# Optimization experiments

Measured on AMD Instinct MI355X. Metric: run time of the kernel, lower is better.

Reference implementation:

```python
import jax, jax.numpy as jnp
import numpy as np

U, B, I, D = 50000, 20000, 40000, 64
E_UI, E_UB, E_UBX, E_AGG = 1000000, 600000, 800000, 300000
EPS = 1e-8


def _bip_graph(rng, nA, nB, nE):
    """Symmetric Laplacian-normalized bipartite graph as directed COO edge list."""
    r = rng.integers(0, nA, nE)
    c = rng.integers(0, nB, nE)
    deg_r = np.bincount(r, minlength=nA).astype(np.float32)
    deg_c = np.bincount(c, minlength=nB).astype(np.float32)
    v = (1.0 / (np.sqrt(deg_r[r]) + EPS)) * (1.0 / (np.sqrt(deg_c[c]) + EPS))
    rows = np.concatenate([r, c + nA])
    cols = np.concatenate([c + nA, r])
    vals = np.concatenate([v, v]).astype(np.float32)
    return np.stack([rows, cols]).astype(np.int32), vals


def setup_inputs() -> dict:
    rng = np.random.default_rng(0)
    ui_idx, ui_val = _bip_graph(rng, U, I, E_UI)
    ub_idx, ub_val = _bip_graph(rng, U, B, E_UB)
    ubx_idx, ubx_val = _bip_graph(rng, U, B, E_UBX)  # ingredient-augmented u-b graph
    # bundle aggregation graph: row-normalized B x I (bi graph)
    br = rng.integers(0, B, E_AGG)
    bc = rng.integers(0, I, E_AGG)
    bdeg = np.bincount(br, minlength=B).astype(np.float32)
    agg_val = (1.0 / np.maximum(bdeg[br], 1.0)).astype(np.float32)
    agg_idx = np.stack([br, bc]).astype(np.int32)
    key = jax.random.key(0)
    ku, kb, ki = jax.random.split(key, 3)
    s = np.sqrt(2.0 / (U + D)).astype(np.float32)  # xavier-normal-ish scale
    return {
        "users_feature": jax.random.normal(ku, (U, D), jnp.float32) * 0.02,
        "bundles_feature": jax.random.normal(kb, (B, D), jnp.float32) * 0.02,
        "items_feature": jax.random.normal(ki, (I, D), jnp.float32) * 0.02,
        "ui_idx": jnp.asarray(ui_idx), "ui_val": jnp.asarray(ui_val),
        "ub_idx": jnp.asarray(ub_idx), "ub_val": jnp.asarray(ub_val),
        "ubx_idx": jnp.asarray(ubx_idx), "ubx_val": jnp.asarray(ubx_val),
        "agg_idx": jnp.asarray(agg_idx), "agg_val": jnp.asarray(agg_val),
        "num_layers": 2,
    }


def _spmm(idx, val, x, n_out):
    # y[r] += val[e] * x[c] for each edge e=(r,c)
    return jax.ops.segment_sum(val[:, None] * x[idx[1]], idx[0], num_segments=n_out)


def _l2norm(x):
    n = jnp.sqrt(jnp.sum(x * x, axis=1, keepdims=True))
    return x / jnp.maximum(n, 1e-12)


def _one_propagate(idx, val, A_feat, B_feat, num_layers):
    feats = jnp.concatenate([A_feat, B_feat], axis=0)
    n = feats.shape[0]
    acc = feats  # layer 0 raw
    f = feats
    for i in range(num_layers):
        f = _spmm(idx, val, f, n) / (i + 2)
        acc = acc + _l2norm(f)
    return acc[: A_feat.shape[0]], acc[A_feat.shape[0]:]


def reference(users_feature, bundles_feature, items_feature, ui_idx, ui_val,
              ub_idx, ub_val, ubx_idx, ubx_val, agg_idx, agg_val, num_layers):
    # item-level propagation over user-item graph
    IL_u, IL_i = _one_propagate(ui_idx, ui_val, users_feature, items_feature, num_layers)
    IL_b = _spmm(agg_idx, agg_val, IL_i, bundles_feature.shape[0])  # bundle agg from items
    # bundle-level propagation over user-bundle graph
    BL_u, BL_b = _one_propagate(ub_idx, ub_val, users_feature, bundles_feature, num_layers)
    # ingredient-augmented user-bundle propagation
    XL_u, XL_b = _one_propagate(ubx_idx, ubx_val, users_feature, bundles_feature, num_layers)
    # pack all representations: [3*U + 3*B, D]
    return jnp.concatenate([IL_u, BL_u, XL_u, IL_b, BL_b, XL_b], axis=0)
```

## Files before the change

### kernel.cpp

```cpp
#include <hip/hip_runtime.h>

#define D 64
constexpr int U_ = 50000, B_ = 20000, I_ = 40000;
constexpr int RPB  = 128;
constexpr int MAXB = 708;
constexpr int PTILE = 8192;

constexpr int NBU = 390;
constexpr int CAPU_UI = 3584, CAPB_UI = 4352;
constexpr int CAPA    = 2560;
constexpr int CAPU_UB = 2432, CAPB_UB = 4864;
constexpr int CAPU_UX = 2944, CAPB_UX = 6272;

__device__ __forceinline__ int g_nbU(int seg) { return seg == 1 ? 0 : NBU; }
__device__ __forceinline__ int g_capU(int seg) {
    switch (seg) { case 0: return CAPU_UI; case 1: return CAPA;
                   case 2: return CAPU_UB; default: return CAPU_UX; }
}
__device__ __forceinline__ int g_capB(int seg) {
    switch (seg) { case 0: return CAPB_UI; case 1: return CAPA;
                   case 2: return CAPB_UB; default: return CAPB_UX; }
}
__device__ __forceinline__ int bbase(int seg, int b) {
    int nbU = g_nbU(seg);
    return (b <= nbU) ? b * g_capU(seg)
                      : nbU * g_capU(seg) + (b - nbU) * g_capB(seg);
}

__device__ __forceinline__ unsigned short f2bf(float f) {
    unsigned int u = __float_as_uint(f);
    return (unsigned short)((u + 0x7FFFu + ((u >> 16) & 1u)) >> 16);
}

struct BuildP {
    const int *r0, *r1, *r2, *r3;
    int nnz0, nnz1, nnz2, nnz3;
    int G0, G1, G2, G3;
    int nb0, nb1, nb2, nb3;
    int co0, co1, co2, co3;
};

__global__ void __launch_bounds__(256)
k_cnt4(BuildP p, int* __restrict__ cnt) {
    __shared__ int lcnt[MAXB];
    int blk = blockIdx.x, t = threadIdx.x;
    int seg, rel, nnz, G, nbuck, co; const int* rows;
    if (blk < p.G0)                   { seg=0; rel=blk;              rows=p.r0; nnz=p.nnz0; G=p.G0; nbuck=p.nb0; co=p.co0; }
    else if (blk < p.G0+p.G1)         { seg=1; rel=blk-p.G0;         rows=p.r1; nnz=p.nnz1; G=p.G1; nbuck=p.nb1; co=p.co1; }
    else if (blk < p.G0+p.G1+p.G2)    { seg=2; rel=blk-p.G0-p.G1;    rows=p.r2; nnz=p.nnz2; G=p.G2; nbuck=p.nb2; co=p.co2; }
    else                              { seg=3; rel=blk-p.G0-p.G1-p.G2; rows=p.r3; nnz=p.nnz3; G=p.G3; nbuck=p.nb3; co=p.co3; }
    (void)seg;
    for (int i = t; i < nbuck; i += 256) lcnt[i] = 0;
    __syncthreads();
    int e0 = rel * PTILE, e1 = min(e0 + PTILE, nnz);
    int e = e0 + t;
    for (; e + 1792 < e1; e += 2048) {
        int r[8];
        #pragma unroll
        for (int k = 0; k < 8; k++) r[k] = rows[e + k * 256];
        #pragma unroll
        for (int k = 0; k < 8; k++) atomicAdd(&lcnt[r[k] >> 7], 1);
    }
    for (; e < e1; e += 256) atomicAdd(&lcnt[rows[e] >> 7], 1);
    __syncthreads();
    for (int b = t; b < nbuck; b += 256) cnt[co + (size_t)b * G + rel] = lcnt[b];
}

__global__ void __launch_bounds__(256)
k_scan4(BuildP p, int* __restrict__ cnt, int* __restrict__ bktcur) {
    __shared__ int sv[256];
    int bk = blockIdx.x, t = threadIdx.x;
    int seg, rel, G, co;
    if (bk < p.nb0)                    { seg=0; rel=bk;                 G=p.G0; co=p.co0; }
    else if (bk < p.nb0+p.nb1)         { seg=1; rel=bk-p.nb0;           G=p.G1; co=p.co1; }
    else if (bk < p.nb0+p.nb1+p.nb2)   { seg=2; rel=bk-p.nb0-p.nb1;     G=p.G2; co=p.co2; }
    else                               { seg=3; rel=bk-p.nb0-p.nb1-p.nb2; G=p.G3; co=p.co3; }
    int x = (t < G) ? cnt[co + (size_t)rel * G + t] : 0;
    sv[t] = x;
    __syncthreads();
    for (int off = 1; off < 256; off <<= 1) {
        int y = (t >= off) ? sv[t - off] : 0;
        __syncthreads();
        sv[t] += y;
        __syncthreads();
    }
    int bb = bbase(seg, rel);
    if (t < G) cnt[co + (size_t)rel * G + t] = bb + sv[t] - x;
    if (t == 255) bktcur[seg * MAXB + rel] = bb + sv[255];
}

__global__ void __launch_bounds__(256)
k_scat(const int* __restrict__ rows, const int* __restrict__ cols,
       int nnz, int G, int nbuck, int seg,
       const int* __restrict__ cnt, int* __restrict__ ep) {
    __shared__ int lbase[MAXB], lcnt[MAXB], llim[MAXB];
    int t = threadIdx.x, blk = blockIdx.x;
    for (int b = t; b < nbuck; b += 256) {
        lbase[b] = cnt[(size_t)b * G + blk];
        llim[b]  = bbase(seg, b + 1);
        lcnt[b]  = 0;
    }
    __syncthreads();
    int e0 = blk * PTILE, e1 = min(e0 + PTILE, nnz);
    int e = e0 + t;
    for (; e + 1792 < e1; e += 2048) {
        int r[8], c[8];
        #pragma unroll
        for (int k = 0; k < 8; k++) { r[k] = rows[e + k * 256]; c[k] = cols[e + k * 256]; }
        #pragma unroll
        for (int k = 0; k < 8; k++) {
            int b = r[k] >> 7;
            int pos = lbase[b] + atomicAdd(&lcnt[b], 1);
            if (pos < llim[b])
                ep[pos] = ((r[k] & (RPB - 1)) << 17) | c[k];
        }
    }
    for (; e < e1; e += 256) {
        int r = rows[e], c = cols[e];
        int b = r >> 7;
        int pos = lbase[b] + atomicAdd(&lcnt[b], 1);
        if (pos < llim[b])
            ep[pos] = ((r & (RPB - 1)) << 17) | c;
    }
}

__global__ void __launch_bounds__(256)
k_sort(const int* __restrict__ ep, const int* __restrict__ bktcur, int seg,
       int n, int mode, int do_pad, int* __restrict__ ecolS,
       int* __restrict__ rowstart, int* __restrict__ rowend,
       float* __restrict__ scale, int do_stage,
       const float* __restrict__ rawA, const float* __restrict__ rawB_adj,
       ushort* __restrict__ fb) {
    __shared__ int lc[4 * 129];
    __shared__ float sscale[RPB];
    __shared__ int wtot;
    int t = threadIdx.x;
    int b = blockIdx.x;
    int s = bbase(seg, b);
    int e = min(bktcur[b], bbase(seg, b + 1));
    int ne = e - s;
    for (int i = t; i < 4 * 129; i += 256) lc[i] = 0;
    __syncthreads();
    int rep = (t & 3) * 129;
    int i = t;
    for (; i + 768 < ne; i += 1024) {
        int p0 = ep[s + i], p1 = ep[s + i + 256], p2 = ep[s + i + 512], p3 = ep[s + i + 768];
        atomicAdd(&lc[rep + (p0 >> 17)], 1); atomicAdd(&lc[rep + (p1 >> 17)], 1);
        atomicAdd(&lc[rep + (p2 >> 17)], 1); atomicAdd(&lc[rep + (p3 >> 17)], 1);
    }
    for (; i < ne; i += 256) { int p = ep[s + i]; atomicAdd(&lc[rep + (p >> 17)], 1); }
    __syncthreads();
    int c_t = 0, pc_t = 0, v = 0;
    if (t < RPB) {
        c_t = lc[t] + lc[129 + t] + lc[258 + t] + lc[387 + t];
        pc_t = do_pad ? ((c_t + 7) & ~7) : c_t;
        v = pc_t;
        for (int off = 1; off < 64; off <<= 1) {
            int y = __shfl_up(v, off, 64);
            if ((t & 63) >= off) v += y;
        }
    }
    if (t == 63) wtot = v;
    __syncthreads();
    if (t >= 64 && t < RPB) v += wtot;
    if (t < RPB) {
        int row = b * RPB + t;
        if (row < n) {
            int st = s + (v - pc_t);
            rowstart[row] = st;
            rowend[row]   = st + pc_t;
            float sc = (mode == 0) ? 1.0f / (sqrtf((float)c_t) + 1e-8f)
                                   : 1.0f / (float)max(c_t, 1);
            scale[row] = sc;
            sscale[t] = sc;
            for (int k = c_t; k < pc_t; k++) ecolS[st + k] = n;
            lc[t] = st;
        } else lc[t] = 0;
    }
    __syncthreads();
    i = t;
    for (; i + 768 < ne; i += 1024) {
        int p0 = ep[s + i], p1 = ep[s + i + 256], p2 = ep[s + i + 512], p3 = ep[s + i + 768];
        int q0 = atomicAdd(&lc[p0 >> 17], 1); ecolS[q0] = p0 & 0x1FFFF;
        int q1 = atomicAdd(&lc[p1 >> 17], 1); ecolS[q1] = p1 & 0x1FFFF;
        int q2 = atomicAdd(&lc[p2 >> 17], 1); ecolS[q2] = p2 & 0x1FFFF;
        int q3 = atomicAdd(&lc[p3 >> 17], 1); ecolS[q3] = p3 & 0x1FFFF;
    }
    for (; i < ne; i += 256) {
        int p = ep[s + i];
        int q = atomicAdd(&lc[p >> 17], 1);
        ecolS[q] = p & 0x1FFFF;
    }
    if (do_stage) {
        int r0 = b * RPB;
        for (int idx = t; idx < RPB * 16; idx += 256) {
            int rl = idx >> 4, q = idx & 15;
            int row = r0 + rl;
            if (row > n) continue;
            ushort4 o;
            if (row == n) {
                o = make_ushort4(0, 0, 0, 0);
            } else {
                float sc = sscale[rl];
                float4 vv = (row < U_) ? ((const float4*)rawA)[(size_t)row * 16 + q]
                                       : ((const float4*)rawB_adj)[(size_t)row * 16 + q];
                o.x = f2bf(vv.x * sc); o.y = f2bf(vv.y * sc);
                o.z = f2bf(vv.z * sc); o.w = f2bf(vv.w * sc);
            }
            ((ushort4*)fb)[(size_t)row * 16 + q] = o;
        }
    }
}

__global__ void __launch_bounds__(256)
k_layer(const int* __restrict__ rowstart, const int* __restrict__ rowend,
        const int* __restrict__ ecol,
        const float* __restrict__ scale, int n, int zrow,
        const ushort* __restrict__ x, float inv,
        const float* __restrict__ rawA, const float* __restrict__ rawB_adj,
        ushort* __restrict__ fout, int write_f, int init,
        float* __restrict__ accA, float* __restrict__ accB) {
    if (write_f && blockIdx.x == 0 && threadIdx.x < 16)
        ((ushort4*)(fout + ((size_t)zrow << 6)))[threadIdx.x] = make_ushort4(0, 0, 0, 0);
    const int lane = threadIdx.x & 63;
    const int qtr  = lane >> 4;
    const int ql   = lane & 15;
    const int g = ql >> 3, q = ql & 7;
    int rowA = (blockIdx.x << 4) + ((threadIdx.x >> 6) << 2);
    if (rowA >= n) return;
    int row = rowA + qtr;
    int s = 0, e = 0;
    if (row < n) { s = rowstart[row]; e = rowend[row]; }
    float a0=0.f,a1=0.f,a2=0.f,a3=0.f,a4=0.f,a5=0.f,a6=0.f,a7=0.f;
    const uint4* __restrict__ xb = (const uint4*)x;

#define LDQ(m, vv) { int c_ = __shfl(cj, (qtr << 4) + ((m) << 1) + g, 64); \
                     vv = xb[((size_t)(unsigned)c_ << 3) + (unsigned)q]; }
#define ACCQ(vv) { \
    a0 += __uint_as_float(vv.x << 16); a1 += __uint_as_float(vv.x & 0xFFFF0000u); \
    a2 += __uint_as_float(vv.y << 16); a3 += __uint_as_float(vv.y & 0xFFFF0000u); \
    a4 += __uint_as_float(vv.z << 16); a5 += __uint_as_float(vv.z & 0xFFFF0000u); \
    a6 += __uint_as_float(vv.w << 16); a7 += __uint_as_float(vv.w & 0xFFFF0000u); }

    for (int base = s; base < e; base += 16) {
        int jn = e - base;
        int cj = ecol[base + ql];
        uint4 v0, v1, v2, v3, v4, v5, v6, v7;
        if (jn >= 16) {
            LDQ(0, v0); LDQ(1, v1); LDQ(2, v2); LDQ(3, v3);
            LDQ(4, v4); ACCQ(v0);
            LDQ(5, v5); ACCQ(v1);
            LDQ(6, v6); ACCQ(v2);
            LDQ(7, v7); ACCQ(v3);
            ACCQ(v4); ACCQ(v5); ACCQ(v6); ACCQ(v7);
        } else {
            LDQ(0, v0); LDQ(1, v1); LDQ(2, v2); LDQ(3, v3);
            ACCQ(v0); ACCQ(v1); ACCQ(v2); ACCQ(v3);
        }
    }
#undef LDQ
#undef ACCQ
#define RED(aa) { aa += __shfl_xor(aa, 8, 64); }
    RED(a0) RED(a1) RED(a2) RED(a3) RED(a4) RED(a5) RED(a6) RED(a7)
#undef RED
    float srow = (row < n) ? scale[row] : 0.f;
    float mlt = srow * inv;
    float w0=a0*mlt, w1=a1*mlt, w2=a2*mlt, w3=a3*mlt;
    float w4=a4*mlt, w5=a5*mlt, w6=a6*mlt, w7=a7*mlt;
    float sq = w0*w0 + w1*w1 + w2*w2 + w3*w3 + w4*w4 + w5*w5 + w6*w6 + w7*w7;
    sq += __shfl_xor(sq, 1, 64); sq += __shfl_xor(sq, 2, 64); sq += __shfl_xor(sq, 4, 64);
    float rn = 1.0f / fmaxf(sqrtf(sq), 1e-12f);
    if (row < n && g == 0) {
        size_t o = ((size_t)row << 6) + ((unsigned)q << 3);
        if (write_f) {
            unsigned p0 = (unsigned)f2bf(w0*srow) | ((unsigned)f2bf(w1*srow) << 16);
            unsigned p1 = (unsigned)f2bf(w2*srow) | ((unsigned)f2bf(w3*srow) << 16);
            unsigned p2 = (unsigned)f2bf(w4*srow) | ((unsigned)f2bf(w5*srow) << 16);
            unsigned p3 = (unsigned)f2bf(w6*srow) | ((unsigned)f2bf(w7*srow) << 16);
            *(uint4*)(fout + o) = make_uint4(p0, p1, p2, p3);
        }
        float r0=w0*rn, r1=w1*rn, r2=w2*rn, r3=w3*rn;
        float r4=w4*rn, r5=w5*rn, r6=w6*rn, r7=w7*rn;
        float* p = (row < U_) ? accA + o : accB + (o - ((size_t)U_ << 6));
        float4 c0, c1;
        if (init) {
            const float4* rp = (const float4*)((row < U_) ? rawA : rawB_adj)
                               + ((size_t)row << 4) + ((unsigned)q << 1);
            c0 = rp[0]; c1 = rp[1];
        } else {
            c0 = ((const float4*)p)[0]; c1 = ((const float4*)p)[1];
        }
        ((float4*)p)[0] = make_float4(c0.x + r0, c0.y + r1, c0.z + r2, c0.w + r3);
        ((float4*)p)[1] = make_float4(c1.x + r4, c1.y + r5, c1.z + r6, c1.w + r7);
    }
}

__global__ void k_spmm_csr(const int* __restrict__ rowstart, const int* __restrict__ rowend,
                           const int* __restrict__ ecol,
                           const float* __restrict__ rs, int n,
                           const float* __restrict__ x, float* __restrict__ y) {
    int row = (blockIdx.x << 2) + (threadIdx.x >> 6);
    if (row >= n) return;
    int lane = threadIdx.x & 63;
    int s = rowstart[row], e = rowend[row];
    float acc = 0.f;
    for (int base = s; base < e; base += 64) {
        int jn = e - base; if (jn > 64) jn = 64;
        int li = base + (lane < jn ? lane : jn - 1);
        int cj = ecol[li];
        int j = 0;
        for (; j + 8 <= jn; j += 8) {
            int c0 = __shfl(cj, j + 0, 64), c1 = __shfl(cj, j + 1, 64);
            int c2 = __shfl(cj, j + 2, 64), c3 = __shfl(cj, j + 3, 64);
            int c4 = __shfl(cj, j + 4, 64), c5 = __shfl(cj, j + 5, 64);
            int c6 = __shfl(cj, j + 6, 64), c7 = __shfl(cj, j + 7, 64);
            float v0 = x[(size_t)c0 * D + lane], v1 = x[(size_t)c1 * D + lane];
            float v2 = x[(size_t)c2 * D + lane], v3 = x[(size_t)c3 * D + lane];
            float v4 = x[(size_t)c4 * D + lane], v5 = x[(size_t)c5 * D + lane];
            float v6 = x[(size_t)c6 * D + lane], v7 = x[(size_t)c7 * D + lane];
            acc += ((v0 + v1) + (v2 + v3)) + ((v4 + v5) + (v6 + v7));
        }
        for (; j < jn; j++) {
            int c = __shfl(cj, j, 64);
            acc += x[(size_t)c * D + lane];
        }
    }
    y[(size_t)row * D + lane] = acc * rs[row];
}

extern "C" void kernel_launch(void* const* d_in, const int* in_sizes, int n_in,
                              void* d_out, int out_size, void* d_ws, size_t ws_size,
                              hipStream_t stream) {
    const float* users   = (const float*)d_in[0];
    const float* bundles = (const float*)d_in[1];
    const float* items   = (const float*)d_in[2];
    const int*   ui_idx  = (const int*)d_in[3];
    const int*   ub_idx  = (const int*)d_in[5];
    const int*   ubx_idx = (const int*)d_in[7];
    const int*   agg_idx = (const int*)d_in[9];
    const int ui_nnz  = in_sizes[4];
    const int ub_nnz  = in_sizes[6];
    const int ubx_nnz = in_sizes[8];
    const int agg_nnz = in_sizes[10];

    float* out = (float*)d_out;
    const size_t rowf = (size_t)D;

    const int NROWPAD = 90004;
    const int EPMAX   = 547 * 6144;
    ushort* fb16    = (ushort*)d_ws;
    float*  acc_itm = (float*)(fb16 + (size_t)(90001) * D + 32);
    float*  scale   = acc_itm + (size_t)I_ * D;
    int*    ep      = (int*)(scale + NROWPAD);
    ushort* gb16    = (ushort*)ep;
    int*    ecolS   = ep + EPMAX;
    int*    rowstart= ecolS + EPMAX;
    int*    rowend  = rowstart + NROWPAD;
    int*    bktcur  = rowend + NROWPAD;
    int*    cnt     = ep + 2950000;

    float* out_IL_u = out;
    float* out_BL_u = out + (size_t)U_ * rowf;
    float* out_XL_u = out + (size_t)2 * U_ * rowf;
    float* out_IL_b = out + (size_t)3 * U_ * rowf;
    float* out_BL_b = out + (size_t)3 * U_ * rowf + (size_t)B_ * rowf;
    float* out_XL_b = out + (size_t)3 * U_ * rowf + (size_t)2 * B_ * rowf;

    BuildP P;
    P.r0 = ui_idx;  P.nnz0 = ui_nnz;  P.G0 = (ui_nnz  + PTILE - 1) / PTILE;  P.nb0 = 704;
    P.r1 = agg_idx; P.nnz1 = agg_nnz; P.G1 = (agg_nnz + PTILE - 1) / PTILE;  P.nb1 = 157;
    P.r2 = ub_idx;  P.nnz2 = ub_nnz;  P.G2 = (ub_nnz  + PTILE - 1) / PTILE;  P.nb2 = 547;
    P.r3 = ubx_idx; P.nnz3 = ubx_nnz; P.G3 = (ubx_nnz + PTILE - 1) / PTILE;  P.nb3 = 547;
    P.co0 = 0;
    P.co1 = P.co0 + P.nb0 * P.G0;
    P.co2 = P.co1 + P.nb1 * P.G1;
    P.co3 = P.co2 + P.nb2 * P.G2;
    int Gsum  = P.G0 + P.G1 + P.G2 + P.G3;
    int nbsum = P.nb0 + P.nb1 + P.nb2 + P.nb3;
    hipLaunchKernelGGL(k_cnt4,  dim3(Gsum),  dim3(256), 0, stream, P, cnt);
    hipLaunchKernelGGL(k_scan4, dim3(nbsum), dim3(256), 0, stream, P, cnt, bktcur);

    auto build = [&](const int* idxp, int nnz, int n, int mode, int do_pad,
                     int do_stage, const float* A, const float* Badj,
                     int seg, int G, int co) {
        int nbuck = (n + RPB - 1) / RPB;
        hipLaunchKernelGGL(k_scat, dim3(G), dim3(256), 0, stream,
                           idxp, idxp + nnz, nnz, G, nbuck, seg, cnt + co, ep);
        hipLaunchKernelGGL(k_sort, dim3(nbuck), dim3(256), 0, stream,
                           ep, bktcur + seg * MAXB, seg, n, mode, do_pad, ecolS,
                           rowstart, rowend, scale, do_stage, A, Badj, fb16);
    };

    auto propagate = [&](const int* idxp, int nnz, int seg, int G, int co,
                         const float* Bfeat, int nB, float* accA, float* accB) {
        const int n = U_ + nB;
        const float* Badj = Bfeat - (size_t)U_ * rowf;
        build(idxp, nnz, n, 0, 1, 1, users, Badj, seg, G, co);
        hipLaunchKernelGGL(k_layer, dim3((n + 15) / 16), dim3(256), 0, stream,
                           rowstart, rowend, ecolS, scale, n, n, fb16, 0.5f,
                           users, Badj, gb16, 1, 1, accA, accB);
        hipLaunchKernelGGL(k_layer, dim3((n + 15) / 16), dim3(256), 0, stream,
                           rowstart, rowend, ecolS, scale, n, n, gb16, 1.0f / 3.0f,
                           users, Badj, (ushort*)nullptr, 0, 0, accA, accB);
    };

    propagate(ui_idx, ui_nnz, 0, P.G0, P.co0, items, I_, out_IL_u, acc_itm);

    build(agg_idx, agg_nnz, B_, 1, 0, 0, users, users, 1, P.G1, P.co1);
    hipLaunchKernelGGL(k_spmm_csr, dim3((B_ + 3) / 4), dim3(256), 0, stream,
                       rowstart, rowend, ecolS, scale, B_, acc_itm, out_IL_b);

    propagate(ub_idx, ub_nnz, 2, P.G2, P.co2, bundles, B_, out_BL_u, out_BL_b);

    propagate(ubx_idx, ubx_nnz, 3, P.G3, P.co3, bundles, B_, out_XL_u, out_XL_b);
}
```

Baseline: 463.3 us.

## Batch all four graph builds and propagations into combined multi-graph launches

Gives each graph its own workspace regions, so that the scatter, sort and layer kernels for all graphs can run as single grouped launches instead of a serialized per-graph sequence. The kernel count drops from about 17 to 8, which removes launch gaps and lets small grids fill the GPU. The cost is a larger workspace, plus a per-block search to find which graph the block belongs to. When the workspace is too small, the code falls back to the old per-graph sequence.

```diff
diff --git a/kernel.cpp b/kernel.cpp
--- a/kernel.cpp
+++ b/kernel.cpp
@@ -11,6 +11,11 @@
 constexpr int CAPA    = 2560;
 constexpr int CAPU_UB = 2432, CAPB_UB = 4864;
 constexpr int CAPU_UX = 2944, CAPB_UX = 6272;
+constexpr int EXT_UI = NBU * CAPU_UI + 314 * CAPB_UI;
+constexpr int EXT_AG = 157 * CAPA;
+constexpr int EXT_UB = NBU * CAPU_UB + 157 * CAPB_UB;
+constexpr int EXT_UX = NBU * CAPU_UX + 157 * CAPB_UX;
+constexpr long long EXT_SUM = (long long)EXT_UI + EXT_AG + EXT_UB + EXT_UX;
 
 __device__ __forceinline__ int g_nbU(int seg) { return seg == 1 ? 0 : NBU; }
 __device__ __forceinline__ int g_capU(int seg) {
@@ -32,27 +37,27 @@
     return (unsigned short)((u + 0x7FFFu + ((u >> 16) & 1u)) >> 16);
 }
 
-struct BuildP {
-    const int *r0, *r1, *r2, *r3;
-    int nnz0, nnz1, nnz2, nnz3;
-    int G0, G1, G2, G3;
-    int nb0, nb1, nb2, nb3;
-    int co0, co1, co2, co3;
+struct GD {
+    const int* rows; const int* cols;
+    int* ep; int* cnt; int* bktcur;
+    int* ecol; int* rowstart; int* rowend; float* scale;
+    const float* rawA; const float* rawB_adj;
+    ushort* fb;
+    int nnz, G, nbuck, seg, n, mode, do_pad, do_stage;
 };
-
-__global__ void __launch_bounds__(256)
-k_cnt4(BuildP p, int* __restrict__ cnt) {
+struct GB4 { GD g[4]; int ng; int Gpre[5]; int nbpre[5]; };
+
+__global__ void __launch_bounds__(256) k_cntB(GB4 P) {
     __shared__ int lcnt[MAXB];
     int blk = blockIdx.x, t = threadIdx.x;
-    int seg, rel, nnz, G, nbuck, co; const int* rows;
-    if (blk < p.G0)                   { seg=0; rel=blk;              rows=p.r0; nnz=p.nnz0; G=p.G0; nbuck=p.nb0; co=p.co0; }
-    else if (blk < p.G0+p.G1)         { seg=1; rel=blk-p.G0;         rows=p.r1; nnz=p.nnz1; G=p.G1; nbuck=p.nb1; co=p.co1; }
-    else if (blk < p.G0+p.G1+p.G2)    { seg=2; rel=blk-p.G0-p.G1;    rows=p.r2; nnz=p.nnz2; G=p.G2; nbuck=p.nb2; co=p.co2; }
-    else                              { seg=3; rel=blk-p.G0-p.G1-p.G2; rows=p.r3; nnz=p.nnz3; G=p.G3; nbuck=p.nb3; co=p.co3; }
-    (void)seg;
-    for (int i = t; i < nbuck; i += 256) lcnt[i] = 0;
-    __syncthreads();
-    int e0 = rel * PTILE, e1 = min(e0 + PTILE, nnz);
+    int gi = 0;
+    while (gi + 1 < P.ng && blk >= P.Gpre[gi + 1]) gi++;
+    const GD& d = P.g[gi];
+    int rel = blk - P.Gpre[gi];
+    const int* __restrict__ rows = d.rows;
+    for (int i = t; i < d.nbuck; i += 256) lcnt[i] = 0;
+    __syncthreads();
+    int e0 = rel * PTILE, e1 = min(e0 + PTILE, d.nnz);
     int e = e0 + t;
     for (; e + 1792 < e1; e += 2048) {
         int r[8];
@@ -63,19 +68,17 @@
     }
     for (; e < e1; e += 256) atomicAdd(&lcnt[rows[e] >> 7], 1);
     __syncthreads();
-    for (int b = t; b < nbuck; b += 256) cnt[co + (size_t)b * G + rel] = lcnt[b];
-}
-
-__global__ void __launch_bounds__(256)
-k_scan4(BuildP p, int* __restrict__ cnt, int* __restrict__ bktcur) {
+    for (int b = t; b < d.nbuck; b += 256) d.cnt[(size_t)b * d.G + rel] = lcnt[b];
+}
+
+__global__ void __launch_bounds__(256) k_scanB(GB4 P) {
     __shared__ int sv[256];
     int bk = blockIdx.x, t = threadIdx.x;
-    int seg, rel, G, co;
-    if (bk < p.nb0)                    { seg=0; rel=bk;                 G=p.G0; co=p.co0; }
-    else if (bk < p.nb0+p.nb1)         { seg=1; rel=bk-p.nb0;           G=p.G1; co=p.co1; }
-    else if (bk < p.nb0+p.nb1+p.nb2)   { seg=2; rel=bk-p.nb0-p.nb1;     G=p.G2; co=p.co2; }
-    else                               { seg=3; rel=bk-p.nb0-p.nb1-p.nb2; G=p.G3; co=p.co3; }
-    int x = (t < G) ? cnt[co + (size_t)rel * G + t] : 0;
+    int gi = 0;
+    while (gi + 1 < P.ng && bk >= P.nbpre[gi + 1]) gi++;
+    const GD& d = P.g[gi];
+    int rel = bk - P.nbpre[gi];
+    int x = (t < d.G) ? d.cnt[(size_t)rel * d.G + t] : 0;
     sv[t] = x;
     __syncthreads();
     for (int off = 1; off < 256; off <<= 1) {
@@ -84,24 +87,28 @@
         sv[t] += y;
         __syncthreads();
     }
-    int bb = bbase(seg, rel);
-    if (t < G) cnt[co + (size_t)rel * G + t] = bb + sv[t] - x;
-    if (t == 255) bktcur[seg * MAXB + rel] = bb + sv[255];
-}
-
-__global__ void __launch_bounds__(256)
-k_scat(const int* __restrict__ rows, const int* __restrict__ cols,
-       int nnz, int G, int nbuck, int seg,
-       const int* __restrict__ cnt, int* __restrict__ ep) {
+    int bb = bbase(d.seg, rel);
+    if (t < d.G) d.cnt[(size_t)rel * d.G + t] = bb + sv[t] - x;
+    if (t == 255) d.bktcur[rel] = bb + sv[255];
+}
+
+__global__ void __launch_bounds__(256) k_scatB(GB4 P) {
     __shared__ int lbase[MAXB], lcnt[MAXB], llim[MAXB];
-    int t = threadIdx.x, blk = blockIdx.x;
-    for (int b = t; b < nbuck; b += 256) {
-        lbase[b] = cnt[(size_t)b * G + blk];
-        llim[b]  = bbase(seg, b + 1);
+    int blk = blockIdx.x, t = threadIdx.x;
+    int gi = 0;
+    while (gi + 1 < P.ng && blk >= P.Gpre[gi + 1]) gi++;
+    const GD& d = P.g[gi];
+    int rel = blk - P.Gpre[gi];
+    const int* __restrict__ rows = d.rows;
+    const int* __restrict__ cols = d.cols;
+    int* __restrict__ ep = d.ep;
+    for (int b = t; b < d.nbuck; b += 256) {
+        lbase[b] = d.cnt[(size_t)b * d.G + rel];
+        llim[b]  = bbase(d.seg, b + 1);
         lcnt[b]  = 0;
     }
     __syncthreads();
-    int e0 = blk * PTILE, e1 = min(e0 + PTILE, nnz);
+    int e0 = rel * PTILE, e1 = min(e0 + PTILE, d.nnz);
     int e = e0 + t;
     for (; e + 1792 < e1; e += 2048) {
         int r[8], c[8];
@@ -124,27 +131,26 @@
     }
 }
 
-__global__ void __launch_bounds__(256)
-k_sort(const int* __restrict__ ep, const int* __restrict__ bktcur, int seg,
-       int n, int mode, int do_pad, int* __restrict__ ecolS,
-       int* __restrict__ rowstart, int* __restrict__ rowend,
-       float* __restrict__ scale, int do_stage,
-       const float* __restrict__ rawA, const float* __restrict__ rawB_adj,
-       ushort* __restrict__ fb) {
+__global__ void __launch_bounds__(256) k_sortB(GB4 P) {
     __shared__ int lc[4 * 129];
     __shared__ float sscale[RPB];
     __shared__ int wtot;
-    int t = threadIdx.x;
-    int b = blockIdx.x;
-    int s = bbase(seg, b);
-    int e = min(bktcur[b], bbase(seg, b + 1));
+    int bk = blockIdx.x, t = threadIdx.x;
+    int gi = 0;
+    while (gi + 1 < P.ng && bk >= P.nbpre[gi + 1]) gi++;
+    const GD& d = P.g[gi];
+    int b = bk - P.nbpre[gi];
+    const int* __restrict__ ep = d.ep;
+    int* __restrict__ ecol = d.ecol;
+    int s = bbase(d.seg, b);
+    int e = min(d.bktcur[b], bbase(d.seg, b + 1));
     int ne = e - s;
     for (int i = t; i < 4 * 129; i += 256) lc[i] = 0;
     __syncthreads();
     int rep = (t & 3) * 129;
     int i = t;
     for (; i + 768 < ne; i += 1024) {
-        int p0 = ep[s + i], p1 = ep[s + i + 256], p2 = ep[s + i + 512], p3 = ep[s + i + 768];
+        int p0 = ep[s+i], p1 = ep[s+i+256], p2 = ep[s+i+512], p3 = ep[s+i+768];
         atomicAdd(&lc[rep + (p0 >> 17)], 1); atomicAdd(&lc[rep + (p1 >> 17)], 1);
         atomicAdd(&lc[rep + (p2 >> 17)], 1); atomicAdd(&lc[rep + (p3 >> 17)], 1);
     }
@@ -153,7 +159,7 @@
     int c_t = 0, pc_t = 0, v = 0;
     if (t < RPB) {
         c_t = lc[t] + lc[129 + t] + lc[258 + t] + lc[387 + t];
-        pc_t = do_pad ? ((c_t + 7) & ~7) : c_t;
+        pc_t = d.do_pad ? ((c_t + 7) & ~7) : c_t;
         v = pc_t;
         for (int off = 1; off < 64; off <<= 1) {
             int y = __shfl_up(v, off, 64);
@@ -165,75 +171,85 @@
     if (t >= 64 && t < RPB) v += wtot;
     if (t < RPB) {
         int row = b * RPB + t;
-        if (row < n) {
+        if (row < d.n) {
             int st = s + (v - pc_t);
-            rowstart[row] = st;
-            rowend[row]   = st + pc_t;
-            float sc = (mode == 0) ? 1.0f / (sqrtf((float)c_t) + 1e-8f)
-                                   : 1.0f / (float)max(c_t, 1);
-            scale[row] = sc;
+            d.rowstart[row] = st;
+            d.rowend[row]   = st + pc_t;
+            float sc = (d.mode == 0) ? 1.0f / (sqrtf((float)c_t) + 1e-8f)
+                                     : 1.0f / (float)max(c_t, 1);
+            d.scale[row] = sc;
             sscale[t] = sc;
-            for (int k = c_t; k < pc_t; k++) ecolS[st + k] = n;
+            for (int k = c_t; k < pc_t; k++) ecol[st + k] = d.n;
             lc[t] = st;
         } else lc[t] = 0;
     }
     __syncthreads();
     i = t;
     for (; i + 768 < ne; i += 1024) {
-        int p0 = ep[s + i], p1 = ep[s + i + 256], p2 = ep[s + i + 512], p3 = ep[s + i + 768];
-        int q0 = atomicAdd(&lc[p0 >> 17], 1); ecolS[q0] = p0 & 0x1FFFF;
-        int q1 = atomicAdd(&lc[p1 >> 17], 1); ecolS[q1] = p1 & 0x1FFFF;
-        int q2 = atomicAdd(&lc[p2 >> 17], 1); ecolS[q2] = p2 & 0x1FFFF;
-        int q3 = atomicAdd(&lc[p3 >> 17], 1); ecolS[q3] = p3 & 0x1FFFF;
+        int p0 = ep[s+i], p1 = ep[s+i+256], p2 = ep[s+i+512], p3 = ep[s+i+768];
+        int q0 = atomicAdd(&lc[p0 >> 17], 1); ecol[q0] = p0 & 0x1FFFF;
+        int q1 = atomicAdd(&lc[p1 >> 17], 1); ecol[q1] = p1 & 0x1FFFF;
+        int q2 = atomicAdd(&lc[p2 >> 17], 1); ecol[q2] = p2 & 0x1FFFF;
+        int q3 = atomicAdd(&lc[p3 >> 17], 1); ecol[q3] = p3 & 0x1FFFF;
     }
     for (; i < ne; i += 256) {
         int p = ep[s + i];
         int q = atomicAdd(&lc[p >> 17], 1);
-        ecolS[q] = p & 0x1FFFF;
-    }
-    if (do_stage) {
+        ecol[q] = p & 0x1FFFF;
+    }
+    if (d.do_stage) {
         int r0 = b * RPB;
         for (int idx = t; idx < RPB * 16; idx += 256) {
             int rl = idx >> 4, q = idx & 15;
             int row = r0 + rl;
-            if (row > n) continue;
+            if (row > d.n) continue;
             ushort4 o;
-            if (row == n) {
+            if (row == d.n) {
                 o = make_ushort4(0, 0, 0, 0);
             } else {
                 float sc = sscale[rl];
-                float4 vv = (row < U_) ? ((const float4*)rawA)[(size_t)row * 16 + q]
-                                       : ((const float4*)rawB_adj)[(size_t)row * 16 + q];
+                float4 vv = (row < U_) ? ((const float4*)d.rawA)[(size_t)row * 16 + q]
+                                       : ((const float4*)d.rawB_adj)[(size_t)row * 16 + q];
                 o.x = f2bf(vv.x * sc); o.y = f2bf(vv.y * sc);
                 o.z = f2bf(vv.z * sc); o.w = f2bf(vv.w * sc);
             }
-            ((ushort4*)fb)[(size_t)row * 16 + q] = o;
-        }
-    }
-}
-
-__global__ void __launch_bounds__(256)
-k_layer(const int* __restrict__ rowstart, const int* __restrict__ rowend,
-        const int* __restrict__ ecol,
-        const float* __restrict__ scale, int n, int zrow,
-        const ushort* __restrict__ x, float inv,
-        const float* __restrict__ rawA, const float* __restrict__ rawB_adj,
-        ushort* __restrict__ fout, int write_f, int init,
-        float* __restrict__ accA, float* __restrict__ accB) {
-    if (write_f && blockIdx.x == 0 && threadIdx.x < 16)
-        ((ushort4*)(fout + ((size_t)zrow << 6)))[threadIdx.x] = make_ushort4(0, 0, 0, 0);
+            ((ushort4*)d.fb)[(size_t)row * 16 + q] = o;
+        }
+    }
+}
+
+struct LD {
+    const int* rowstart; const int* rowend; const float* scale;
+    const int* ecol; const ushort* x; ushort* fout;
+    const float* rawA; const float* rawB_adj;
+    float* accA; float* accB;
+    float inv; int n, write_f, init;
+};
+struct LB3 { LD l[3]; int nl; int qpre[4]; };
+
+__global__ void __launch_bounds__(256) k_layerB(LB3 P) {
+    int blk = blockIdx.x;
+    int gi = 0;
+    while (gi + 1 < P.nl && blk >= P.qpre[gi + 1]) gi++;
+    const LD& d = P.l[gi];
+    int rel = blk - P.qpre[gi];
+    if (d.write_f && rel == 0 && threadIdx.x < 16)
+        ((ushort4*)(d.fout + ((size_t)d.n << 6)))[threadIdx.x] = make_ushort4(0, 0, 0, 0);
+    const int* __restrict__ rowstart = d.rowstart;
+    const int* __restrict__ rowend   = d.rowend;
+    const int* __restrict__ ecol     = d.ecol;
+    const float* __restrict__ scale  = d.scale;
+    const uint4* __restrict__ xb = (const uint4*)d.x;
     const int lane = threadIdx.x & 63;
     const int qtr  = lane >> 4;
     const int ql   = lane & 15;
     const int g = ql >> 3, q = ql & 7;
-    int rowA = (blockIdx.x << 4) + ((threadIdx.x >> 6) << 2);
-    if (rowA >= n) return;
+    int rowA = (rel << 4) + ((threadIdx.x >> 6) << 2);
+    if (rowA >= d.n) return;
     int row = rowA + qtr;
     int s = 0, e = 0;
-    if (row < n) { s = rowstart[row]; e = rowend[row]; }
+    if (row < d.n) { s = rowstart[row]; e = rowend[row]; }
     float a0=0.f,a1=0.f,a2=0.f,a3=0.f,a4=0.f,a5=0.f,a6=0.f,a7=0.f;
-    const uint4* __restrict__ xb = (const uint4*)x;
-
 #define LDQ(m, vv) { int c_ = __shfl(cj, (qtr << 4) + ((m) << 1) + g, 64); \
                      vv = xb[((size_t)(unsigned)c_ << 3) + (unsigned)q]; }
 #define ACCQ(vv) { \
@@ -241,7 +257,6 @@
     a2 += __uint_as_float(vv.y << 16); a3 += __uint_as_float(vv.y & 0xFFFF0000u); \
     a4 += __uint_as_float(vv.z << 16); a5 += __uint_as_float(vv.z & 0xFFFF0000u); \
     a6 += __uint_as_float(vv.w << 16); a7 += __uint_as_float(vv.w & 0xFFFF0000u); }
-
     for (int base = s; base < e; base += 16) {
         int jn = e - base;
         int cj = ecol[base + ql];
@@ -263,28 +278,28 @@
 #define RED(aa) { aa += __shfl_xor(aa, 8, 64); }
     RED(a0) RED(a1) RED(a2) RED(a3) RED(a4) RED(a5) RED(a6) RED(a7)
 #undef RED
-    float srow = (row < n) ? scale[row] : 0.f;
-    float mlt = srow * inv;
+    float srow = (row < d.n) ? scale[row] : 0.f;
+    float mlt = srow * d.inv;
     float w0=a0*mlt, w1=a1*mlt, w2=a2*mlt, w3=a3*mlt;
     float w4=a4*mlt, w5=a5*mlt, w6=a6*mlt, w7=a7*mlt;
     float sq = w0*w0 + w1*w1 + w2*w2 + w3*w3 + w4*w4 + w5*w5 + w6*w6 + w7*w7;
     sq += __shfl_xor(sq, 1, 64); sq += __shfl_xor(sq, 2, 64); sq += __shfl_xor(sq, 4, 64);
     float rn = 1.0f / fmaxf(sqrtf(sq), 1e-12f);
-    if (row < n && g == 0) {
+    if (row < d.n && g == 0) {
         size_t o = ((size_t)row << 6) + ((unsigned)q << 3);
-        if (write_f) {
+        if (d.write_f) {
             unsigned p0 = (unsigned)f2bf(w0*srow) | ((unsigned)f2bf(w1*srow) << 16);
             unsigned p1 = (unsigned)f2bf(w2*srow) | ((unsigned)f2bf(w3*srow) << 16);
             unsigned p2 = (unsigned)f2bf(w4*srow) | ((unsigned)f2bf(w5*srow) << 16);
             unsigned p3 = (unsigned)f2bf(w6*srow) | ((unsigned)f2bf(w7*srow) << 16);
-            *(uint4*)(fout + o) = make_uint4(p0, p1, p2, p3);
+            *(uint4*)(d.fout + o) = make_uint4(p0, p1, p2, p3);
         }
         float r0=w0*rn, r1=w1*rn, r2=w2*rn, r3=w3*rn;
         float r4=w4*rn, r5=w5*rn, r6=w6*rn, r7=w7*rn;
-        float* p = (row < U_) ? accA + o : accB + (o - ((size_t)U_ << 6));
+        float* p = (row < U_) ? d.accA + o : d.accB + (o - ((size_t)U_ << 6));
         float4 c0, c1;
-        if (init) {
-            const float4* rp = (const float4*)((row < U_) ? rawA : rawB_adj)
+        if (d.init) {
+            const float4* rp = (const float4*)((row < U_) ? d.rawA : d.rawB_adj)
                                + ((size_t)row << 4) + ((unsigned)q << 1);
             c0 = rp[0]; c1 = rp[1];
         } else {
@@ -345,20 +360,6 @@
 
     float* out = (float*)d_out;
     const size_t rowf = (size_t)D;
-
-    const int NROWPAD = 90004;
-    const int EPMAX   = 547 * 6144;
-    ushort* fb16    = (ushort*)d_ws;
-    float*  acc_itm = (float*)(fb16 + (size_t)(90001) * D + 32);
-    float*  scale   = acc_itm + (size_t)I_ * D;
-    int*    ep      = (int*)(scale + NROWPAD);
-    ushort* gb16    = (ushort*)ep;
-    int*    ecolS   = ep + EPMAX;
-    int*    rowstart= ecolS + EPMAX;
-    int*    rowend  = rowstart + NROWPAD;
-    int*    bktcur  = rowend + NROWPAD;
-    int*    cnt     = ep + 2950000;
-
     float* out_IL_u = out;
     float* out_BL_u = out + (size_t)U_ * rowf;
     float* out_XL_u = out + (size_t)2 * U_ * rowf;
@@ -366,51 +367,158 @@
     float* out_BL_b = out + (size_t)3 * U_ * rowf + (size_t)B_ * rowf;
     float* out_XL_b = out + (size_t)3 * U_ * rowf + (size_t)2 * B_ * rowf;
 
-    BuildP P;
-    P.r0 = ui_idx;  P.nnz0 = ui_nnz;  P.G0 = (ui_nnz  + PTILE - 1) / PTILE;  P.nb0 = 704;
-    P.r1 = agg_idx; P.nnz1 = agg_nnz; P.G1 = (agg_nnz + PTILE - 1) / PTILE;  P.nb1 = 157;
-    P.r2 = ub_idx;  P.nnz2 = ub_nnz;  P.G2 = (ub_nnz  + PTILE - 1) / PTILE;  P.nb2 = 547;
-    P.r3 = ubx_idx; P.nnz3 = ubx_nnz; P.G3 = (ubx_nnz + PTILE - 1) / PTILE;  P.nb3 = 547;
-    P.co0 = 0;
-    P.co1 = P.co0 + P.nb0 * P.G0;
-    P.co2 = P.co1 + P.nb1 * P.G1;
-    P.co3 = P.co2 + P.nb2 * P.G2;
-    int Gsum  = P.G0 + P.G1 + P.G2 + P.G3;
-    int nbsum = P.nb0 + P.nb1 + P.nb2 + P.nb3;
-    hipLaunchKernelGGL(k_cnt4,  dim3(Gsum),  dim3(256), 0, stream, P, cnt);
-    hipLaunchKernelGGL(k_scan4, dim3(nbsum), dim3(256), 0, stream, P, cnt, bktcur);
-
-    auto build = [&](const int* idxp, int nnz, int n, int mode, int do_pad,
-                     int do_stage, const float* A, const float* Badj,
-                     int seg, int G, int co) {
-        int nbuck = (n + RPB - 1) / RPB;
-        hipLaunchKernelGGL(k_scat, dim3(G), dim3(256), 0, stream,
-                           idxp, idxp + nnz, nnz, G, nbuck, seg, cnt + co, ep);
-        hipLaunchKernelGGL(k_sort, dim3(nbuck), dim3(256), 0, stream,
-                           ep, bktcur + seg * MAXB, seg, n, mode, do_pad, ecolS,
-                           rowstart, rowend, scale, do_stage, A, Badj, fb16);
-    };
-
-    auto propagate = [&](const int* idxp, int nnz, int seg, int G, int co,
-                         const float* Bfeat, int nB, float* accA, float* accB) {
-        const int n = U_ + nB;
-        const float* Badj = Bfeat - (size_t)U_ * rowf;
-        build(idxp, nnz, n, 0, 1, 1, users, Badj, seg, G, co);
-        hipLaunchKernelGGL(k_layer, dim3((n + 15) / 16), dim3(256), 0, stream,
-                           rowstart, rowend, ecolS, scale, n, n, fb16, 0.5f,
-                           users, Badj, gb16, 1, 1, accA, accB);
-        hipLaunchKernelGGL(k_layer, dim3((n + 15) / 16), dim3(256), 0, stream,
-                           rowstart, rowend, ecolS, scale, n, n, gb16, 1.0f / 3.0f,
-                           users, Badj, (ushort*)nullptr, 0, 0, accA, accB);
-    };
-
-    propagate(ui_idx, ui_nnz, 0, P.G0, P.co0, items, I_, out_IL_u, acc_itm);
-
-    build(agg_idx, agg_nnz, B_, 1, 0, 0, users, users, 1, P.G1, P.co1);
-    hipLaunchKernelGGL(k_spmm_csr, dim3((B_ + 3) / 4), dim3(256), 0, stream,
-                       rowstart, rowend, ecolS, scale, B_, acc_itm, out_IL_b);
-
-    propagate(ub_idx, ub_nnz, 2, P.G2, P.co2, bundles, B_, out_BL_u, out_BL_b);
-
-    propagate(ubx_idx, ubx_nnz, 3, P.G3, P.co3, bundles, B_, out_XL_u, out_XL_b);
-}
+    const int G0 = (ui_nnz  + PTILE - 1) / PTILE;
+    const int G1 = (agg_nnz + PTILE - 1) / PTILE;
+    const int G2 = (ub_nnz  + PTILE - 1) / PTILE;
+    const int G3 = (ubx_nnz + PTILE - 1) / PTILE;
+    const int NB0 = 704, NB1 = 157, NB2 = 547, NB3 = 547;
+    const size_t co0 = 0, co1 = (size_t)NB0 * G0, co2 = co1 + (size_t)NB1 * G1,
+                 co3 = co2 + (size_t)NB2 * G2, cntInts = co3 + (size_t)NB3 * G3;
+    const int nU = U_ + I_, nB2g = U_ + B_;
+
+    const int* rowsArr[4] = { ui_idx, agg_idx, ub_idx, ubx_idx };
+    const int nnzArr[4]   = { ui_nnz, agg_nnz, ub_nnz, ubx_nnz };
+    const int GArr[4]     = { G0, G1, G2, G3 };
+    const int nbArr[4]    = { NB0, NB1, NB2, NB3 };
+    const int nArr[4]     = { nU, B_, nB2g, nB2g };
+    const int modeArr[4]  = { 0, 1, 0, 0 };
+    const int padArr[4]   = { 1, 0, 1, 1 };
+    const int stgArr[4]   = { 1, 0, 1, 1 };
+    const size_t coArr[4] = { co0, co1, co2, co3 };
+    const float* rawBArr[4] = { items - (size_t)U_ * rowf, users,
+                                bundles - (size_t)U_ * rowf, bundles - (size_t)U_ * rowf };
+
+    const size_t fbBytes  = 230003ull * 128;
+    const size_t accBytes = 40001ull * 256;
+    const size_t ecBytes  = (size_t)EXT_SUM * 4;
+    const size_t rsBytes  = 250016ull * 4;
+    const size_t bkBytes  = 4ull * MAXB * 4;
+    const size_t epcnt    = (size_t)EXT_SUM * 4 + cntInts * 4;
+    const size_t tailB    = epcnt > fbBytes ? epcnt : fbBytes;
+    const size_t reqA     = fbBytes + accBytes + ecBytes + 3 * rsBytes + bkBytes + tailB + 4096;
+
+    GB4 P{};
+    P.ng = 4;
+    P.Gpre[0] = 0; P.nbpre[0] = 0;
+    for (int i = 0; i < 4; i++) { P.Gpre[i+1] = P.Gpre[i] + GArr[i]; P.nbpre[i+1] = P.nbpre[i] + nbArr[i]; }
+
+    if (ws_size >= reqA) {
+        char* w = (char*)d_ws;
+        ushort* fbA   = (ushort*)w;                 w += fbBytes;
+        float* accI   = (float*)w;                  w += accBytes;
+        int*   ecolA  = (int*)w;                    w += ecBytes;
+        int*   rsA    = (int*)w;                    w += rsBytes;
+        int*   reA    = (int*)w;                    w += rsBytes;
+        float* scA    = (float*)w;                  w += rsBytes;
+        int*   bkA    = (int*)w;                    w += bkBytes;
+        int*   epA    = (int*)w;
+        int*   cntA   = epA + EXT_SUM;
+        ushort* gbA   = (ushort*)epA;
+
+        const size_t epoff[4] = { 0, (size_t)EXT_UI, (size_t)EXT_UI + EXT_AG,
+                                  (size_t)EXT_UI + EXT_AG + EXT_UB };
+        const size_t roff[4]  = { 0, 90004, 110008, 180012 };
+        const size_t fboff[4] = { 0, 0, 90001ull * 64, 160002ull * 64 };
+
+        for (int i = 0; i < 4; i++) {
+            GD& d = P.g[i];
+            d.rows = rowsArr[i]; d.cols = rowsArr[i] + nnzArr[i];
+            d.ep = epA + epoff[i]; d.cnt = cntA + coArr[i]; d.bktcur = bkA + i * MAXB;
+            d.ecol = ecolA + epoff[i];
+            d.rowstart = rsA + roff[i]; d.rowend = reA + roff[i]; d.scale = scA + roff[i];
+            d.rawA = users; d.rawB_adj = rawBArr[i];
+            d.fb = (i == 1) ? nullptr : fbA + fboff[i];
+            d.nnz = nnzArr[i]; d.G = GArr[i]; d.nbuck = nbArr[i]; d.seg = i;
+            d.n = nArr[i]; d.mode = modeArr[i]; d.do_pad = padArr[i]; d.do_stage = stgArr[i];
+        }
+        hipLaunchKernelGGL(k_cntB,  dim3(P.Gpre[4]),  dim3(256), 0, stream, P);
+        hipLaunchKernelGGL(k_scanB, dim3(P.nbpre[4]), dim3(256), 0, stream, P);
+        hipLaunchKernelGGL(k_scatB, dim3(P.Gpre[4]),  dim3(256), 0, stream, P);
+        hipLaunchKernelGGL(k_sortB, dim3(P.nbpre[4]), dim3(256), 0, stream, P);
+
+        float* accAArr[3] = { out_IL_u, out_BL_u, out_XL_u };
+        float* accBArr[3] = { accI, out_BL_b, out_XL_b };
+        int gsel[3] = { 0, 2, 3 };
+        LB3 L{};
+        L.nl = 3; L.qpre[0] = 0;
+        for (int j = 0; j < 3; j++) {
+            int i = gsel[j];
+            LD& l = L.l[j];
+            l.rowstart = P.g[i].rowstart; l.rowend = P.g[i].rowend; l.scale = P.g[i].scale;
+            l.ecol = P.g[i].ecol; l.rawA = users; l.rawB_adj = rawBArr[i];
+            l.accA = accAArr[j]; l.accB = accBArr[j];
+            l.n = nArr[i];
+            L.qpre[j + 1] = L.qpre[j] + ((nArr[i] + 15) >> 4);
+        }
+        for (int j = 0; j < 3; j++) {
+            int i = gsel[j];
+            L.l[j].x = fbA + fboff[i]; L.l[j].fout = gbA + fboff[i];
+            L.l[j].inv = 0.5f; L.l[j].write_f = 1; L.l[j].init = 1;
+        }
+        hipLaunchKernelGGL(k_layerB, dim3(L.qpre[3]), dim3(256), 0, stream, L);
+        for (int j = 0; j < 3; j++) {
+            int i = gsel[j];
+            L.l[j].x = gbA + fboff[i]; L.l[j].fout = (ushort*)nullptr;
+            L.l[j].inv = 1.0f / 3.0f; L.l[j].write_f = 0; L.l[j].init = 0;
+        }
+        hipLaunchKernelGGL(k_layerB, dim3(L.qpre[3]), dim3(256), 0, stream, L);
+        hipLaunchKernelGGL(k_spmm_csr, dim3((B_ + 3) / 4), dim3(256), 0, stream,
+                           P.g[1].rowstart, P.g[1].rowend, P.g[1].ecol,
+                           P.g[1].scale, B_, accI, out_IL_b);
+    } else {
+        const int NROWPAD = 90004;
+        const int EPMAX = 547 * 6144;
+        ushort* fb16 = (ushort*)d_ws;
+        float* accI  = (float*)(fb16 + (size_t)90001 * D + 32);
+        float* scB   = accI + (size_t)I_ * D;
+        int* epB     = (int*)(scB + NROWPAD);
+        ushort* gb16 = (ushort*)epB;
+        int* ecolB   = epB + EPMAX;
+        int* rsB     = ecolB + EPMAX;
+        int* reB     = rsB + NROWPAD;
+        int* bkB     = reB + NROWPAD;
+        int* cntB    = epB + 2950000;
+
+        for (int i = 0; i < 4; i++) {
+            GD& d = P.g[i];
+            d.rows = rowsArr[i]; d.cols = rowsArr[i] + nnzArr[i];
+            d.ep = epB; d.cnt = cntB + coArr[i]; d.bktcur = bkB + i * MAXB;
+            d.ecol = ecolB; d.rowstart = rsB; d.rowend = reB; d.scale = scB;
+            d.rawA = users; d.rawB_adj = rawBArr[i];
+            d.fb = fb16;
+            d.nnz = nnzArr[i]; d.G = GArr[i]; d.nbuck = nbArr[i]; d.seg = i;
+            d.n = nArr[i]; d.mode = modeArr[i]; d.do_pad = padArr[i]; d.do_stage = stgArr[i];
+        }
+        hipLaunchKernelGGL(k_cntB,  dim3(P.Gpre[4]),  dim3(256), 0, stream, P);
+        hipLaunchKernelGGL(k_scanB, dim3(P.nbpre[4]), dim3(256), 0, stream, P);
+
+        auto one = [&](int i) {
+            GB4 Q{};
+            Q.ng = 1; Q.g[0] = P.g[i];
+            Q.Gpre[0] = 0; Q.Gpre[1] = GArr[i];
+            Q.nbpre[0] = 0; Q.nbpre[1] = nbArr[i];
+            hipLaunchKernelGGL(k_scatB, dim3(GArr[i]),  dim3(256), 0, stream, Q);
+            hipLaunchKernelGGL(k_sortB, dim3(nbArr[i]), dim3(256), 0, stream, Q);
+        };
+        auto layers = [&](int i, float* accA, float* accB) {
+            LB3 L{};
+            L.nl = 1; L.qpre[0] = 0; L.qpre[1] = (nArr[i] + 15) >> 4;
+            LD& l = L.l[0];
+            l.rowstart = rsB; l.rowend = reB; l.scale = scB; l.ecol = ecolB;
+            l.rawA = users; l.rawB_adj = rawBArr[i];
+            l.accA = accA; l.accB = accB; l.n = nArr[i];
+            l.x = fb16; l.fout = gb16; l.inv = 0.5f; l.write_f = 1; l.init = 1;
+            hipLaunchKernelGGL(k_layerB, dim3(L.qpre[1]), dim3(256), 0, stream, L);
+            l.x = gb16; l.fout = (ushort*)nullptr; l.inv = 1.0f / 3.0f;
+            l.write_f = 0; l.init = 0;
+            hipLaunchKernelGGL(k_layerB, dim3(L.qpre[1]), dim3(256), 0, stream, L);
+        };
+
+        one(0); layers(0, out_IL_u, accI);
+        one(1);
+        hipLaunchKernelGGL(k_spmm_csr, dim3((B_ + 3) / 4), dim3(256), 0, stream,
+                           rsB, reB, ecolB, scB, B_, accI, out_IL_b);
+        one(2); layers(2, out_BL_u, out_BL_b);
+        one(3); layers(3, out_XL_u, out_XL_b);
+    }
+}
```

After: 431.3 us. 6.9% less time.
